# Optimization experiments

Hardware: AMD Instinct MI355X
Metric: run time of the kernel (lower is better)

## Reference

```python
import jax, jax.numpy as jnp
import numpy as np

B, L, D = 8, 2048, 256
D_MODEL = 1024
NUM_SIGNALS = 16
MAX_POSITIONS = 4096
ROLE_OUTPUT = 2  # role id used for the CLS token


def setup_inputs() -> dict:
    key = jax.random.key(0)
    ks = jax.random.split(key, 12)
    emb = jax.random.normal(ks[0], (B, L, D), dtype=jnp.float32)
    pos = jax.random.randint(ks[1], (B, L), 1, MAX_POSITIONS + 1)          # pos >= 1 for real tokens
    sid = jax.random.randint(ks[2], (B, L), 0, NUM_SIGNALS)
    role = jax.random.randint(ks[3], (B, L), 0, 3)
    padding_mask = jax.random.uniform(ks[4], (B, L)) < 0.75                # True = real token
    # learned parameters
    proj_W = jax.random.normal(ks[5], (NUM_SIGNALS, D_MODEL, D), dtype=jnp.float32) * (1.0 / np.sqrt(D))
    proj_b = jax.random.normal(ks[6], (NUM_SIGNALS, D_MODEL), dtype=jnp.float32) * 0.01
    cls_content = jax.random.normal(ks[7], (D_MODEL,), dtype=jnp.float32)
    pos_embed = jax.random.normal(ks[8], (MAX_POSITIONS + 1, D_MODEL), dtype=jnp.float32)
    id_embed = jax.random.normal(ks[9], (NUM_SIGNALS + 1, D_MODEL), dtype=jnp.float32)
    role_embed = jax.random.normal(ks[10], (3, D_MODEL), dtype=jnp.float32)
    return dict(emb=emb, pos=pos, sid=sid, role=role, padding_mask=padding_mask,
                proj_W=proj_W, proj_b=proj_b, cls_content=cls_content,
                pos_embed=pos_embed, id_embed=id_embed, role_embed=role_embed)


def reference(emb, pos, sid, role, padding_mask,
              proj_W, proj_b, cls_content, pos_embed, id_embed, role_embed):
    Bv, Lv, _ = emb.shape
    S, d_model, _ = proj_W.shape
    cls_id = S

    # Grouped per-signal projection: one GEMM per signal id, select per token.
    tokens = jnp.zeros((Bv, Lv, d_model), dtype=emb.dtype)
    for s in range(S):
        proj_s = jnp.einsum('bld,ed->ble', emb, proj_W[s]) + proj_b[s]   # (B, L, d_model)
        keep = ((sid == s) & padding_mask)[..., None]
        tokens = jnp.where(keep, proj_s, tokens)

    # Prepend CLS
    cls = jnp.broadcast_to(cls_content[None, None, :], (Bv, 1, d_model))
    tokens = jnp.concatenate([cls, tokens], axis=1)                       # (B, L+1, d_model)

    pos_full = jnp.concatenate([jnp.zeros((Bv, 1), dtype=pos.dtype), pos], axis=1)
    sid_full = jnp.concatenate([jnp.full((Bv, 1), cls_id, dtype=sid.dtype), sid], axis=1)
    role_full = jnp.concatenate([jnp.full((Bv, 1), ROLE_OUTPUT, dtype=role.dtype), role], axis=1)

    tokens = tokens + pos_embed[pos_full] + id_embed[sid_full] + role_embed[role_full]

    attn_keep = jnp.concatenate([jnp.ones((Bv, 1), dtype=bool), padding_mask], axis=1)
    return tokens, attn_keep
```

## Files before the change

### kernel.cpp

```cpp
#include <hip/hip_runtime.h>
#include <hip/hip_bf16.h>
#include <stdint.h>

#define B_ 8
#define L_ 2048
#define NTOK 16384
#define DK 256
#define DM 1024
#define NS 16
#define LOUT 2049
#define TOK_OUT (B_*LOUT*DM)
#define ATTN_OUT (B_*LOUT)
#define PCAP 2048

typedef unsigned short u16;
typedef unsigned int u32;
typedef __bf16 bf16x8 __attribute__((ext_vector_type(8)));
typedef float f32x4 __attribute__((ext_vector_type(4)));

__device__ inline u32 packbf2(float lo, float hi) {
    u32 a, b;
    __builtin_memcpy(&a, &lo, 4);
    __builtin_memcpy(&b, &hi, 4);
    a = (a + 0x8000u) >> 16;
    b = (b + 0x8000u) & 0xFFFF0000u;
    return a | b;
}

__device__ inline void gll16(const void* g, void* l) {
    __builtin_amdgcn_global_load_lds(
        (const __attribute__((address_space(1))) unsigned int*)g,
        (__attribute__((address_space(3))) unsigned int*)l, 16, 0, 0);
}

#define WS_CUR 0
#define WS_PERM 64
#define WS_MASK (64 + NS * PCAP)
#define A_OFF 262144ULL
#define APAD_ROWS 18432
#define W_OFF (A_OFF + (unsigned long long)APAD_ROWS * 512ULL)
#define WS_NEED (W_OFF + 16384ULL * 512ULL)

__global__ __launch_bounds__(256) void sort_kernel(const unsigned char* __restrict__ mb,
                                                   const int* __restrict__ sid,
                                                   int* __restrict__ wsi) {
    __shared__ int f_c1ge2, f_ge2, f_odd;
    __shared__ int lcnt[NS], gbase[NS];
    int tid = threadIdx.x;
    if (tid == 0) { f_c1ge2 = 0; f_ge2 = 0; f_odd = 0; }
    if (tid < NS) lcnt[tid] = 0;
    __syncthreads();

    int c1ge2 = 0, ge2 = 0, oddnz = 0;
    const u32* mw = (const u32*)mb;
    #pragma unroll
    for (int i = 0; i < 16; i++) {
        u32 x = mw[tid * 16 + i];
        u32 b0 = x & 0xFF, b1 = (x >> 8) & 0xFF, b2 = (x >> 16) & 0xFF, b3 = x >> 24;
        if (b1 >= 2) c1ge2 = 1;
        if (b0 >= 2 || b1 >= 2 || b2 >= 2 || b3 >= 2) ge2 = 1;
        if ((b1 | b3) != 0) oddnz = 1;
    }
    if (c1ge2) atomicOr(&f_c1ge2, 1);
    if (ge2) atomicOr(&f_ge2, 1);
    if (oddnz) atomicOr(&f_odd, 1);
    __syncthreads();

    int width;
    if (f_c1ge2) width = 2;
    else if (f_ge2) width = 4;
    else if (f_odd) width = 1;
    else width = 4;

    int t = blockIdx.x * 256 + tid;
    int m;
    if (width == 1) m = (mb[t] != 0);
    else if (width == 2) m = (((const u16*)mb)[t] != 0);
    else m = (((const u32*)mb)[t] != 0);

    wsi[WS_MASK + t] = m;
    int s = sid[t];
    int lr = 0;
    if (m) lr = atomicAdd(&lcnt[s], 1);
    __syncthreads();
    if (tid < NS) gbase[tid] = atomicAdd(&wsi[WS_CUR + tid], lcnt[tid]);
    __syncthreads();
    if (m) {
        int r = gbase[s] + lr;
        if (r < PCAP) wsi[WS_PERM + s * PCAP + r] = t;
    }
}

__global__ __launch_bounds__(256) void prep_kernel(const float* __restrict__ emb,
                                                   const float* __restrict__ W,
                                                   const int* __restrict__ wsi,
                                                   unsigned char* __restrict__ wsb) {
    int bid = blockIdx.x;
    int tid = threadIdx.x;
    int lane = tid & 63;
    int wv = tid >> 6;
    if (bid < 4608) {
        int cnts[NS], segoff[NS];
        int accp = 0;
        #pragma unroll
        for (int i = 0; i < NS; i++) {
            int c = wsi[WS_CUR + i];
            cnts[i] = c > PCAP ? PCAP : c;
            segoff[i] = accp;
            accp += ((cnts[i] + 127) >> 7) << 7;
        }
        int r = bid * 4 + wv;
        if (r >= accp) return;
        int s = 0;
        #pragma unroll
        for (int i = 1; i < NS; i++) if (r >= segoff[i]) s = i;
        int local = r - segoff[s];
        u16* Ab = (u16*)(wsb + A_OFF);
        uint2 o;
        if (local < cnts[s]) {
            int t = wsi[WS_PERM + s * PCAP + local];
            float4 a = *(const float4*)(emb + (size_t)t * DK + lane * 4);
            o.x = packbf2(a.x, a.y);
            o.y = packbf2(a.z, a.w);
        } else {
            o.x = 0; o.y = 0;
        }
        *(uint2*)(Ab + (size_t)r * DK + lane * 4) = o;
    } else {
        int r = (bid - 4608) * 4 + wv;
        u16* Wb = (u16*)(wsb + W_OFF);
        float4 a = *(const float4*)(W + (size_t)r * DK + lane * 4);
        uint2 o;
        o.x = packbf2(a.x, a.y);
        o.y = packbf2(a.z, a.w);
        *(uint2*)(Wb + (size_t)r * DK + lane * 4) = o;
    }
}

__global__ __launch_bounds__(512, 4) void gemm_big(
    const int* __restrict__ pos, const int* __restrict__ role,
    const float* __restrict__ bias,
    const float* __restrict__ pos_emb, const float* __restrict__ id_emb,
    const float* __restrict__ role_emb,
    const int* __restrict__ wsi, const unsigned char* __restrict__ wsb,
    float* __restrict__ out) {
    __shared__ u16 As[2][128 * 32];
    __shared__ u16 Bs[2][256 * 32];
    __shared__ int toks[128];
    int tid = threadIdx.x;
    int lane = tid & 63;
    int wv = tid >> 6;

    int cnts[NS];
    #pragma unroll
    for (int i = 0; i < NS; i++) {
        int c = wsi[WS_CUR + i];
        cnts[i] = c > PCAP ? PCAP : c;
    }
    int ry = (int)blockIdx.y;
    int s = -1, lrt = 0, seg0 = 0;
    {
        int accp = 0;
        #pragma unroll
        for (int i = 0; i < NS; i++) {
            int rt = (cnts[i] + 127) >> 7;
            if (s < 0) {
                if (ry < rt) { s = i; lrt = ry; seg0 = accp; }
                else ry -= rt;
            }
            accp += rt << 7;
        }
    }
    if (s < 0) return;
    int rowsValid = cnts[s] - lrt * 128;
    if (rowsValid > 128) rowsValid = 128;

    if (tid < 128) toks[tid] = (tid < rowsValid) ? wsi[WS_PERM + s * PCAP + lrt * 128 + tid] : -1;

    int n0 = (int)blockIdx.x * 256;
    const u16* Ab = (const u16*)(wsb + A_OFF) + (size_t)(seg0 + lrt * 128) * DK;
    const u16* Bb = (const u16*)(wsb + W_OFF) + (size_t)(s * DM + n0) * DK;

    int srow = lane >> 2;
    int slseg = lane & 3;

    f32x4 acc[4][4];
    #pragma unroll
    for (int im = 0; im < 4; im++)
        #pragma unroll
        for (int jn = 0; jn < 4; jn++) acc[im][jn] = (f32x4){0.f, 0.f, 0.f, 0.f};

    int wm = wv & 1, wn = wv >> 1;
    int mcol = lane & 15;
    int quad = lane >> 4;

#define STAGE(kc, bf)                                                          \
    {                                                                          \
        int arow = wv * 16 + srow;                                             \
        int ags = (slseg - (arow >> 1)) & 3;                                   \
        gll16(Ab + (size_t)arow * DK + (kc) * 32 + ags * 8,                    \
              &As[bf][wv * 16 * 32]);                                          \
        int brow0 = wv * 16 + srow;                                            \
        int bgs0 = (slseg - (brow0 >> 1)) & 3;                                 \
        gll16(Bb + (size_t)brow0 * DK + (kc) * 32 + bgs0 * 8,                  \
              &Bs[bf][wv * 16 * 32]);                                          \
        int brow1 = 128 + wv * 16 + srow;                                      \
        int bgs1 = (slseg - (brow1 >> 1)) & 3;                                 \
        gll16(Bb + (size_t)brow1 * DK + (kc) * 32 + bgs1 * 8,                  \
              &Bs[bf][(128 + wv * 16) * 32]);                                  \
    }

    STAGE(0, 0)
    #pragma unroll
    for (int kc = 0; kc < 8; ++kc) {
        __syncthreads();
        if (kc < 7) STAGE(kc + 1, (kc + 1) & 1)
        int bf = kc & 1;
        bf16x8 af[4], bfr[4];
        #pragma unroll
        for (int im = 0; im < 4; im++) {
            int row = wm * 64 + im * 16 + mcol;
            int sg = (quad + (row >> 1)) & 3;
            af[im] = *(const bf16x8*)(&As[bf][row * 32 + sg * 8]);
        }
        #pragma unroll
        for (int jn = 0; jn < 4; jn++) {
            int row = wn * 64 + jn * 16 + mcol;
            int sg = (quad + (row >> 1)) & 3;
            bfr[jn] = *(const bf16x8*)(&Bs[bf][row * 32 + sg * 8]);
        }
        #pragma unroll
        for (int im = 0; im < 4; im++)
            #pragma unroll
            for (int jn = 0; jn < 4; jn++)
                acc[im][jn] = __builtin_amdgcn_mfma_f32_16x16x32_bf16(
                    af[im], bfr[jn], acc[im][jn], 0, 0, 0);
    }

    float bc[4];
    #pragma unroll
    for (int jn = 0; jn < 4; jn++) {
        int col = n0 + wn * 64 + jn * 16 + mcol;
        bc[jn] = bias[s * DM + col] + id_emb[s * DM + col];
    }
    #pragma unroll
    for (int im = 0; im < 4; im++) {
        #pragma unroll
        for (int r = 0; r < 4; r++) {
            int rowT = wm * 64 + im * 16 + quad * 4 + r;
            if (rowT >= rowsValid) continue;
            int t = toks[rowT];
            int p = pos[t];
            int ro = role[t];
            int b = t >> 11, l = t & 2047;
            size_t orow = (size_t)(b * LOUT + l + 1) * DM;
            #pragma unroll
            for (int jn = 0; jn < 4; jn++) {
                int col = n0 + wn * 64 + jn * 16 + mcol;
                float val = acc[im][jn][r] + bc[jn]
                    + pos_emb[(size_t)p * DM + col]
                    + role_emb[ro * DM + col];
                out[orow + col] = val;
            }
        }
    }
#undef STAGE
}

__global__ __launch_bounds__(256) void ew_kernel(
    const int* __restrict__ pos, const int* __restrict__ sid,
    const int* __restrict__ role,
    const float* __restrict__ cls, const float* __restrict__ pos_emb,
    const float* __restrict__ id_emb, const float* __restrict__ role_emb,
    const int* __restrict__ wsi, float* __restrict__ out) {
    int bi = blockIdx.x;
    int tid = threadIdx.x;
    int lane = tid & 63;
    int wv = tid >> 6;
    if (bi < NTOK / 4) {
        int t = bi * 4 + wv;
        if (wsi[WS_MASK + t]) return;
        int p = pos[t], sd = sid[t], ro = role[t];
        int b = t >> 11, l = t & 2047;
        size_t orow = (size_t)(b * LOUT + l + 1) * DM;
        #pragma unroll
        for (int it = 0; it < 4; it++) {
            int c = it * 256 + lane * 4;
            float4 a = *(const float4*)(pos_emb + (size_t)p * DM + c);
            float4 d = *(const float4*)(id_emb + (size_t)sd * DM + c);
            float4 e = *(const float4*)(role_emb + (size_t)ro * DM + c);
            float4 o;
            o.x = a.x + d.x + e.x;
            o.y = a.y + d.y + e.y;
            o.z = a.z + d.z + e.z;
            o.w = a.w + d.w + e.w;
            *(float4*)(out + orow + c) = o;
        }
    } else if (bi < NTOK / 4 + 2) {
        int b = (bi - NTOK / 4) * 4 + wv;
        size_t orow = (size_t)(b * LOUT) * DM;
        #pragma unroll
        for (int it = 0; it < 4; it++) {
            int c = it * 256 + lane * 4;
            float4 cc = *(const float4*)(cls + c);
            float4 a = *(const float4*)(pos_emb + c);
            float4 d = *(const float4*)(id_emb + NS * DM + c);
            float4 e = *(const float4*)(role_emb + 2 * DM + c);
            float4 o;
            o.x = cc.x + a.x + d.x + e.x;
            o.y = cc.y + a.y + d.y + e.y;
            o.z = cc.z + a.z + d.z + e.z;
            o.w = cc.w + a.w + d.w + e.w;
            *(float4*)(out + orow + c) = o;
        }
    } else {
        int i = (bi - NTOK / 4 - 2) * 256 + tid;
        if (i < ATTN_OUT) {
            int b = i / LOUT;
            int j = i - b * LOUT;
            float val = (j == 0) ? 1.0f : (float)wsi[WS_MASK + b * L_ + j - 1];
            out[TOK_OUT + i] = val;
        }
    }
}

extern "C" void kernel_launch(void* const* d_in, const int* in_sizes, int n_in,
                              void* d_out, int out_size, void* d_ws, size_t ws_size,
                              hipStream_t stream) {
    const float* emb = (const float*)d_in[0];
    const int* pos = (const int*)d_in[1];
    const int* sid = (const int*)d_in[2];
    const int* role = (const int*)d_in[3];
    const unsigned char* mask = (const unsigned char*)d_in[4];
    const float* W = (const float*)d_in[5];
    const float* bias = (const float*)d_in[6];
    const float* cls = (const float*)d_in[7];
    const float* pos_emb = (const float*)d_in[8];
    const float* id_emb = (const float*)d_in[9];
    const float* role_emb = (const float*)d_in[10];
    float* out = (float*)d_out;
    int* wsi = (int*)d_ws;
    unsigned char* wsb = (unsigned char*)d_ws;

    hipMemsetAsync(wsi, 0, 64 * sizeof(int), stream);
    hipLaunchKernelGGL(sort_kernel, dim3(64), dim3(256), 0, stream, mask, sid, wsi);
    hipLaunchKernelGGL(prep_kernel, dim3(4608 + 4096), dim3(256), 0, stream,
                       emb, W, wsi, wsb);
    hipLaunchKernelGGL(gemm_big, dim3(4, 144), dim3(512), 0, stream,
                       pos, role, bias, pos_emb, id_emb, role_emb, wsi, wsb, out);
    hipLaunchKernelGGL(ew_kernel, dim3(NTOK / 4 + 2 + 65), dim3(256), 0, stream,
                       pos, sid, role, cls, pos_emb, id_emb, role_emb, wsi, out);
}
```

Measured before the change: 161.5 us.

## Make grouped GEMM persistent with cross-tile prefetch of next task

Replaces the 2D grid of per-tile blocks with 256 persistent blocks that stride over (row-tile, column-tile) tasks. While finishing the last k-chunk of one tile, each block computes the next task's descriptor and stages its first A/B chunk, and double-buffers the token index list so the epilogue of one tile overlaps the load of the next. A large padding LDS array and a lower launch-bounds occupancy hint cap residency at about one block per CU, trading occupancy for fewer launches and less tail imbalance.

```diff
diff --git a/kernel.cpp b/kernel.cpp
--- a/kernel.cpp
+++ b/kernel.cpp
@@ -137,7 +137,13 @@
     }
 }
 
-__global__ __launch_bounds__(512, 4) void gemm_big(
+struct Desc {
+    const u16* Ab;
+    const u16* Bb;
+    int s, rv, n0, pidx;
+};
+
+__global__ __launch_bounds__(512, 2) void gemm_big(
     const int* __restrict__ pos, const int* __restrict__ role,
     const float* __restrict__ bias,
     const float* __restrict__ pos_emb, const float* __restrict__ id_emb,
@@ -146,125 +152,160 @@
     float* __restrict__ out) {
     __shared__ u16 As[2][128 * 32];
     __shared__ u16 Bs[2][256 * 32];
-    __shared__ int toks[128];
+    __shared__ int toksbuf[2][128];
+    __shared__ int lds_pad[16384];
+
     int tid = threadIdx.x;
     int lane = tid & 63;
     int wv = tid >> 6;
 
     int cnts[NS];
+    int mtot = 0;
     #pragma unroll
     for (int i = 0; i < NS; i++) {
         int c = wsi[WS_CUR + i];
         cnts[i] = c > PCAP ? PCAP : c;
-    }
-    int ry = (int)blockIdx.y;
-    int s = -1, lrt = 0, seg0 = 0;
-    {
-        int accp = 0;
-        #pragma unroll
-        for (int i = 0; i < NS; i++) {
-            int rt = (cnts[i] + 127) >> 7;
-            if (s < 0) {
-                if (ry < rt) { s = i; lrt = ry; seg0 = accp; }
-                else ry -= rt;
-            }
-            accp += rt << 7;
-        }
-    }
-    if (s < 0) return;
-    int rowsValid = cnts[s] - lrt * 128;
-    if (rowsValid > 128) rowsValid = 128;
-
-    if (tid < 128) toks[tid] = (tid < rowsValid) ? wsi[WS_PERM + s * PCAP + lrt * 128 + tid] : -1;
-
-    int n0 = (int)blockIdx.x * 256;
-    const u16* Ab = (const u16*)(wsb + A_OFF) + (size_t)(seg0 + lrt * 128) * DK;
-    const u16* Bb = (const u16*)(wsb + W_OFF) + (size_t)(s * DM + n0) * DK;
+        mtot += (cnts[i] + 127) >> 7;
+    }
+    if (cnts[0] == -1) ((volatile int*)lds_pad)[0] = 0;
+    int ntasks = mtot * 4;
+    int task = (int)blockIdx.x;
+    if (task >= ntasks) return;
+
+    const u16* Abase = (const u16*)(wsb + A_OFF);
+    const u16* Bbase = (const u16*)(wsb + W_OFF);
+
+#define MKDESC(D, tk)                                                          \
+    {                                                                          \
+        int m = (tk) >> 2;                                                     \
+        D.n0 = ((tk) & 3) << 8;                                                \
+        int s_ = -1, lrt_ = 0, seg0_ = 0, accp_ = 0;                           \
+        _Pragma("unroll")                                                      \
+        for (int i_ = 0; i_ < NS; i_++) {                                      \
+            int rt_ = (cnts[i_] + 127) >> 7;                                   \
+            if (s_ < 0) {                                                      \
+                if (m < rt_) { s_ = i_; lrt_ = m; seg0_ = accp_; }             \
+                else m -= rt_;                                                 \
+            }                                                                  \
+            accp_ += rt_ << 7;                                                 \
+        }                                                                      \
+        D.s = s_;                                                              \
+        int rv_ = cnts[s_] - lrt_ * 128;                                       \
+        D.rv = rv_ > 128 ? 128 : rv_;                                          \
+        D.pidx = s_ * PCAP + lrt_ * 128;                                       \
+        D.Ab = Abase + (size_t)(seg0_ + lrt_ * 128) * DK;                      \
+        D.Bb = Bbase + (size_t)(D.s * DM + D.n0) * DK;                         \
+    }
 
     int srow = lane >> 2;
     int slseg = lane & 3;
 
-    f32x4 acc[4][4];
-    #pragma unroll
-    for (int im = 0; im < 4; im++)
-        #pragma unroll
-        for (int jn = 0; jn < 4; jn++) acc[im][jn] = (f32x4){0.f, 0.f, 0.f, 0.f};
+#define STAGE(D, kc, bf)                                                       \
+    {                                                                          \
+        int arow = wv * 16 + srow;                                             \
+        int ags = (slseg - (arow >> 1)) & 3;                                   \
+        gll16(D.Ab + (size_t)arow * DK + (kc) * 32 + ags * 8,                  \
+              &As[bf][wv * 16 * 32]);                                          \
+        int bgs0 = ags;                                                        \
+        gll16(D.Bb + (size_t)arow * DK + (kc) * 32 + bgs0 * 8,                 \
+              &Bs[bf][wv * 16 * 32]);                                          \
+        int brow1 = 128 + arow;                                                \
+        int bgs1 = (slseg - (brow1 >> 1)) & 3;                                 \
+        gll16(D.Bb + (size_t)brow1 * DK + (kc) * 32 + bgs1 * 8,                \
+              &Bs[bf][(128 + wv * 16) * 32]);                                  \
+    }
+
+    Desc d;
+    MKDESC(d, task)
+    if (tid < 128) toksbuf[0][tid] = (tid < d.rv) ? wsi[WS_PERM + d.pidx + tid] : -1;
 
     int wm = wv & 1, wn = wv >> 1;
     int mcol = lane & 15;
     int quad = lane >> 4;
 
-#define STAGE(kc, bf)                                                          \
-    {                                                                          \
-        int arow = wv * 16 + srow;                                             \
-        int ags = (slseg - (arow >> 1)) & 3;                                   \
-        gll16(Ab + (size_t)arow * DK + (kc) * 32 + ags * 8,                    \
-              &As[bf][wv * 16 * 32]);                                          \
-        int brow0 = wv * 16 + srow;                                            \
-        int bgs0 = (slseg - (brow0 >> 1)) & 3;                                 \
-        gll16(Bb + (size_t)brow0 * DK + (kc) * 32 + bgs0 * 8,                  \
-              &Bs[bf][wv * 16 * 32]);                                          \
-        int brow1 = 128 + wv * 16 + srow;                                      \
-        int bgs1 = (slseg - (brow1 >> 1)) & 3;                                 \
-        gll16(Bb + (size_t)brow1 * DK + (kc) * 32 + bgs1 * 8,                  \
-              &Bs[bf][(128 + wv * 16) * 32]);                                  \
-    }
-
-    STAGE(0, 0)
-    #pragma unroll
-    for (int kc = 0; kc < 8; ++kc) {
-        __syncthreads();
-        if (kc < 7) STAGE(kc + 1, (kc + 1) & 1)
-        int bf = kc & 1;
-        bf16x8 af[4], bfr[4];
+    int buf = 0, tp = 0;
+    STAGE(d, 0, 0)
+
+    while (true) {
+        f32x4 acc[4][4];
+        #pragma unroll
+        for (int im = 0; im < 4; im++)
+            #pragma unroll
+            for (int jn = 0; jn < 4; jn++) acc[im][jn] = (f32x4){0.f, 0.f, 0.f, 0.f};
+
+        int ntask = task + 256;
+        bool have = ntask < ntasks;
+        Desc nd = d;
+
+        #pragma unroll
+        for (int kc = 0; kc < 8; ++kc) {
+            __syncthreads();
+            int nb = buf ^ 1;
+            if (kc < 7) {
+                STAGE(d, kc + 1, nb)
+            } else if (have) {
+                MKDESC(nd, ntask)
+                STAGE(nd, 0, nb)
+            }
+            bf16x8 af[4], bfr[4];
+            #pragma unroll
+            for (int im = 0; im < 4; im++) {
+                int row = wm * 64 + im * 16 + mcol;
+                int sg = (quad + (row >> 1)) & 3;
+                af[im] = *(const bf16x8*)(&As[buf][row * 32 + sg * 8]);
+            }
+            #pragma unroll
+            for (int jn = 0; jn < 4; jn++) {
+                int row = wn * 64 + jn * 16 + mcol;
+                int sg = (quad + (row >> 1)) & 3;
+                bfr[jn] = *(const bf16x8*)(&Bs[buf][row * 32 + sg * 8]);
+            }
+            #pragma unroll
+            for (int im = 0; im < 4; im++)
+                #pragma unroll
+                for (int jn = 0; jn < 4; jn++)
+                    acc[im][jn] = __builtin_amdgcn_mfma_f32_16x16x32_bf16(
+                        af[im], bfr[jn], acc[im][jn], 0, 0, 0);
+            buf = nb;
+        }
+
+        if (have && tid < 128)
+            toksbuf[tp ^ 1][tid] = (tid < nd.rv) ? wsi[WS_PERM + nd.pidx + tid] : -1;
+
+        float bc[4];
+        #pragma unroll
+        for (int jn = 0; jn < 4; jn++) {
+            int col = d.n0 + wn * 64 + jn * 16 + mcol;
+            bc[jn] = bias[d.s * DM + col] + id_emb[d.s * DM + col];
+        }
         #pragma unroll
         for (int im = 0; im < 4; im++) {
-            int row = wm * 64 + im * 16 + mcol;
-            int sg = (quad + (row >> 1)) & 3;
-            af[im] = *(const bf16x8*)(&As[bf][row * 32 + sg * 8]);
-        }
-        #pragma unroll
-        for (int jn = 0; jn < 4; jn++) {
-            int row = wn * 64 + jn * 16 + mcol;
-            int sg = (quad + (row >> 1)) & 3;
-            bfr[jn] = *(const bf16x8*)(&Bs[bf][row * 32 + sg * 8]);
-        }
-        #pragma unroll
-        for (int im = 0; im < 4; im++)
-            #pragma unroll
-            for (int jn = 0; jn < 4; jn++)
-                acc[im][jn] = __builtin_amdgcn_mfma_f32_16x16x32_bf16(
-                    af[im], bfr[jn], acc[im][jn], 0, 0, 0);
-    }
-
-    float bc[4];
-    #pragma unroll
-    for (int jn = 0; jn < 4; jn++) {
-        int col = n0 + wn * 64 + jn * 16 + mcol;
-        bc[jn] = bias[s * DM + col] + id_emb[s * DM + col];
-    }
-    #pragma unroll
-    for (int im = 0; im < 4; im++) {
-        #pragma unroll
-        for (int r = 0; r < 4; r++) {
-            int rowT = wm * 64 + im * 16 + quad * 4 + r;
-            if (rowT >= rowsValid) continue;
-            int t = toks[rowT];
-            int p = pos[t];
-            int ro = role[t];
-            int b = t >> 11, l = t & 2047;
-            size_t orow = (size_t)(b * LOUT + l + 1) * DM;
-            #pragma unroll
-            for (int jn = 0; jn < 4; jn++) {
-                int col = n0 + wn * 64 + jn * 16 + mcol;
-                float val = acc[im][jn][r] + bc[jn]
-                    + pos_emb[(size_t)p * DM + col]
-                    + role_emb[ro * DM + col];
-                out[orow + col] = val;
+            #pragma unroll
+            for (int r = 0; r < 4; r++) {
+                int rowT = wm * 64 + im * 16 + quad * 4 + r;
+                if (rowT >= d.rv) continue;
+                int t = toksbuf[tp][rowT];
+                int p = pos[t];
+                int ro = role[t];
+                int b = t >> 11, l = t & 2047;
+                size_t orow = (size_t)(b * LOUT + l + 1) * DM;
+                #pragma unroll
+                for (int jn = 0; jn < 4; jn++) {
+                    int col = d.n0 + wn * 64 + jn * 16 + mcol;
+                    float val = acc[im][jn][r] + bc[jn]
+                        + pos_emb[(size_t)p * DM + col]
+                        + role_emb[ro * DM + col];
+                    out[orow + col] = val;
+                }
             }
         }
+        if (!have) return;
+        d = nd;
+        task = ntask;
+        tp ^= 1;
     }
 #undef STAGE
+#undef MKDESC
 }
 
 __global__ __launch_bounds__(256) void ew_kernel(
@@ -346,7 +387,7 @@
     hipLaunchKernelGGL(sort_kernel, dim3(64), dim3(256), 0, stream, mask, sid, wsi);
     hipLaunchKernelGGL(prep_kernel, dim3(4608 + 4096), dim3(256), 0, stream,
                        emb, W, wsi, wsb);
-    hipLaunchKernelGGL(gemm_big, dim3(4, 144), dim3(512), 0, stream,
+    hipLaunchKernelGGL(gemm_big, dim3(256), dim3(512), 0, stream,
                        pos, role, bias, pos_emb, id_emb, role_emb, wsi, wsb, out);
     hipLaunchKernelGGL(ew_kernel, dim3(NTOK / 4 + 2 + 65), dim3(256), 0, stream,
                        pos, sid, role, cls, pos_emb, id_emb, role_emb, wsi, out);
```

After: 174.8 us. +8.2%, slower.

## Convert pos_embed to bf16 in prep and remap GEMM tiles per XCD

Applied to the files above, without the earlier changes.

The prep kernel now also converts the pos_embed table to bf16 in workspace, and the GEMM epilogue gathers positional rows from that half-size copy instead of the fp32 table. The GEMM launch becomes a 1D grid of 576 blocks whose index is remapped so each XCD (blockIdx & 7) handles a contiguous range of M tiles across all four N tiles, aiming to improve L2 reuse of A tiles and the gathered rows. The trade is an extra 4097x1024 conversion pass every call and bf16 rounding of the positional term, which changes output precision slightly.

```diff
diff --git a/kernel.cpp b/kernel.cpp
--- a/kernel.cpp
+++ b/kernel.cpp
@@ -18,6 +18,13 @@
 typedef __bf16 bf16x8 __attribute__((ext_vector_type(8)));
 typedef float f32x4 __attribute__((ext_vector_type(4)));
 
+__device__ inline float bf2f(u16 u) {
+    u32 x = ((u32)u) << 16;
+    float f;
+    __builtin_memcpy(&f, &x, 4);
+    return f;
+}
+
 __device__ inline u32 packbf2(float lo, float hi) {
     u32 a, b;
     __builtin_memcpy(&a, &lo, 4);
@@ -39,7 +46,8 @@
 #define A_OFF 262144ULL
 #define APAD_ROWS 18432
 #define W_OFF (A_OFF + (unsigned long long)APAD_ROWS * 512ULL)
-#define WS_NEED (W_OFF + 16384ULL * 512ULL)
+#define PE_OFF (W_OFF + 16384ULL * 512ULL)
+#define WS_NEED (PE_OFF + 4097ULL * 1024ULL * 2ULL)
 
 __global__ __launch_bounds__(256) void sort_kernel(const unsigned char* __restrict__ mb,
                                                    const int* __restrict__ sid,
@@ -93,6 +101,7 @@
 
 __global__ __launch_bounds__(256) void prep_kernel(const float* __restrict__ emb,
                                                    const float* __restrict__ W,
+                                                   const float* __restrict__ pos_emb,
                                                    const int* __restrict__ wsi,
                                                    unsigned char* __restrict__ wsb) {
     int bid = blockIdx.x;
@@ -126,7 +135,7 @@
             o.x = 0; o.y = 0;
         }
         *(uint2*)(Ab + (size_t)r * DK + lane * 4) = o;
-    } else {
+    } else if (bid < 4608 + 4096) {
         int r = (bid - 4608) * 4 + wv;
         u16* Wb = (u16*)(wsb + W_OFF);
         float4 a = *(const float4*)(W + (size_t)r * DK + lane * 4);
@@ -134,14 +143,22 @@
         o.x = packbf2(a.x, a.y);
         o.y = packbf2(a.z, a.w);
         *(uint2*)(Wb + (size_t)r * DK + lane * 4) = o;
+    } else {
+        int r = bid - (4608 + 4096);
+        u16* Pb = (u16*)(wsb + PE_OFF);
+        int c = tid * 4;
+        float4 a = *(const float4*)(pos_emb + (size_t)r * DM + c);
+        uint2 o;
+        o.x = packbf2(a.x, a.y);
+        o.y = packbf2(a.z, a.w);
+        *(uint2*)(Pb + (size_t)r * DM + c) = o;
     }
 }
 
 __global__ __launch_bounds__(512, 4) void gemm_big(
     const int* __restrict__ pos, const int* __restrict__ role,
     const float* __restrict__ bias,
-    const float* __restrict__ pos_emb, const float* __restrict__ id_emb,
-    const float* __restrict__ role_emb,
+    const float* __restrict__ id_emb, const float* __restrict__ role_emb,
     const int* __restrict__ wsi, const unsigned char* __restrict__ wsb,
     float* __restrict__ out) {
     __shared__ u16 As[2][128 * 32];
@@ -152,12 +169,24 @@
     int wv = tid >> 6;
 
     int cnts[NS];
+    int mtot = 0;
     #pragma unroll
     for (int i = 0; i < NS; i++) {
         int c = wsi[WS_CUR + i];
         cnts[i] = c > PCAP ? PCAP : c;
-    }
-    int ry = (int)blockIdx.y;
+        mtot += (cnts[i] + 127) >> 7;
+    }
+    int bi = (int)blockIdx.x;
+    int xcd = bi & 7;
+    int j = bi >> 3;
+    int m_lo = (xcd * mtot) >> 3;
+    int m_hi = ((xcd + 1) * mtot) >> 3;
+    int cm = m_hi - m_lo;
+    if (cm <= 0 || j >= cm * 4) return;
+    int nt = j / cm;
+    int m = m_lo + (j - nt * cm);
+    int n0 = nt << 8;
+
     int s = -1, lrt = 0, seg0 = 0;
     {
         int accp = 0;
@@ -165,8 +194,8 @@
         for (int i = 0; i < NS; i++) {
             int rt = (cnts[i] + 127) >> 7;
             if (s < 0) {
-                if (ry < rt) { s = i; lrt = ry; seg0 = accp; }
-                else ry -= rt;
+                if (m < rt) { s = i; lrt = m; seg0 = accp; }
+                else m -= rt;
             }
             accp += rt << 7;
         }
@@ -177,9 +206,9 @@
 
     if (tid < 128) toks[tid] = (tid < rowsValid) ? wsi[WS_PERM + s * PCAP + lrt * 128 + tid] : -1;
 
-    int n0 = (int)blockIdx.x * 256;
     const u16* Ab = (const u16*)(wsb + A_OFF) + (size_t)(seg0 + lrt * 128) * DK;
     const u16* Bb = (const u16*)(wsb + W_OFF) + (size_t)(s * DM + n0) * DK;
+    const u16* Pb = (const u16*)(wsb + PE_OFF);
 
     int srow = lane >> 2;
     int slseg = lane & 3;
@@ -200,11 +229,9 @@
         int ags = (slseg - (arow >> 1)) & 3;                                   \
         gll16(Ab + (size_t)arow * DK + (kc) * 32 + ags * 8,                    \
               &As[bf][wv * 16 * 32]);                                          \
-        int brow0 = wv * 16 + srow;                                            \
-        int bgs0 = (slseg - (brow0 >> 1)) & 3;                                 \
-        gll16(Bb + (size_t)brow0 * DK + (kc) * 32 + bgs0 * 8,                  \
+        gll16(Bb + (size_t)arow * DK + (kc) * 32 + ags * 8,                    \
               &Bs[bf][wv * 16 * 32]);                                          \
-        int brow1 = 128 + wv * 16 + srow;                                      \
+        int brow1 = 128 + arow;                                                \
         int bgs1 = (slseg - (brow1 >> 1)) & 3;                                 \
         gll16(Bb + (size_t)brow1 * DK + (kc) * 32 + bgs1 * 8,                  \
               &Bs[bf][(128 + wv * 16) * 32]);                                  \
@@ -254,11 +281,12 @@
             int ro = role[t];
             int b = t >> 11, l = t & 2047;
             size_t orow = (size_t)(b * LOUT + l + 1) * DM;
+            const u16* prow = Pb + (size_t)p * DM;
             #pragma unroll
             for (int jn = 0; jn < 4; jn++) {
                 int col = n0 + wn * 64 + jn * 16 + mcol;
                 float val = acc[im][jn][r] + bc[jn]
-                    + pos_emb[(size_t)p * DM + col]
+                    + bf2f(prow[col])
                     + role_emb[ro * DM + col];
                 out[orow + col] = val;
             }
@@ -344,10 +372,10 @@
 
     hipMemsetAsync(wsi, 0, 64 * sizeof(int), stream);
     hipLaunchKernelGGL(sort_kernel, dim3(64), dim3(256), 0, stream, mask, sid, wsi);
-    hipLaunchKernelGGL(prep_kernel, dim3(4608 + 4096), dim3(256), 0, stream,
-                       emb, W, wsi, wsb);
-    hipLaunchKernelGGL(gemm_big, dim3(4, 144), dim3(512), 0, stream,
-                       pos, role, bias, pos_emb, id_emb, role_emb, wsi, wsb, out);
+    hipLaunchKernelGGL(prep_kernel, dim3(4608 + 4096 + 4097), dim3(256), 0, stream,
+                       emb, W, pos_emb, wsi, wsb);
+    hipLaunchKernelGGL(gemm_big, dim3(576), dim3(512), 0, stream,
+                       pos, role, bias, id_emb, role_emb, wsi, wsb, out);
     hipLaunchKernelGGL(ew_kernel, dim3(NTOK / 4 + 2 + 65), dim3(256), 0, stream,
                        pos, sid, role, cls, pos_emb, id_emb, role_emb, wsi, out);
 }
```

Result: faster. 155.5 us (-3.8%).
